# Performance work log

Measured on AMD Instinct MI355X. Metric: run time of the kernel, lower is better.

## Reference

```python
import jax, jax.numpy as jnp
import numpy as np

# --- constants (match init_kwargs / input_specs) ---
N_NODES = 32768   # total nodes
N_EDGES = 262144  # total edges (avg degree 8)
B = 512           # number of graphs
D = 64            # node feature / hidden dim (scalar irreps width)
DE = 16           # edge attribute dim
NEXP = 8          # num_experts
K = 2             # top-k


def setup_inputs() -> dict:
    key = jax.random.key(0)
    ks = jax.random.split(key, 20)
    x = jax.random.normal(ks[0], (N_NODES, D), dtype=jnp.float32)
    edge_src = jax.random.randint(ks[1], (N_EDGES,), 0, N_NODES, dtype=jnp.int32)
    edge_dst = jax.random.randint(ks[2], (N_EDGES,), 0, N_NODES, dtype=jnp.int32)
    edge_attr = jax.random.normal(ks[3], (N_EDGES, DE), dtype=jnp.float32)
    # sorted graph ids, every graph non-empty (64 nodes each)
    batch = jnp.repeat(jnp.arange(B, dtype=jnp.int32), N_NODES // B)
    s = 1.0 / np.sqrt(D)
    se = 1.0 / np.sqrt(DE)
    # embedding GNN params
    emb_We = jax.random.normal(ks[4], (DE, D), dtype=jnp.float32) * se
    emb_W1 = jax.random.normal(ks[5], (D, D), dtype=jnp.float32) * s
    emb_W2 = jax.random.normal(ks[6], (D, D), dtype=jnp.float32) * s
    emb_b = jnp.zeros((D,), dtype=jnp.float32)
    # gating network
    Wg = jax.random.normal(ks[7], (D, NEXP), dtype=jnp.float32) * s
    bg = jnp.zeros((NEXP,), dtype=jnp.float32)
    # stacked expert params [NEXP, ...]
    ex_We = jax.random.normal(ks[8], (NEXP, DE, D), dtype=jnp.float32) * se
    ex_W1 = jax.random.normal(ks[9], (NEXP, D, D), dtype=jnp.float32) * s
    ex_W2 = jax.random.normal(ks[10], (NEXP, D, D), dtype=jnp.float32) * s
    ex_b = jnp.zeros((NEXP, D), dtype=jnp.float32)
    ex_Wout = jax.random.normal(ks[11], (NEXP, D, 1), dtype=jnp.float32) * s
    ex_bout = jnp.zeros((NEXP, 1), dtype=jnp.float32)
    return {
        "x": x, "edge_attr": edge_attr,
        "emb_We": emb_We, "emb_W1": emb_W1, "emb_W2": emb_W2, "emb_b": emb_b,
        "Wg": Wg, "bg": bg,
        "ex_We": ex_We, "ex_W1": ex_W1, "ex_W2": ex_W2, "ex_b": ex_b,
        "ex_Wout": ex_Wout, "ex_bout": ex_bout,
        "edge_src": edge_src, "edge_dst": edge_dst, "batch": batch,
    }


def _gnn_embed(x, edge_attr, We, W1, W2, b, src, dst, batch):
    # edge-gated messages: gather x[src], modulate by projected edge attrs, scatter to dst
    msg = x[src] * (edge_attr @ We)                          # [E, D]
    agg = jax.ops.segment_sum(msg, dst, num_segments=N_NODES)  # [N, D]
    h = jax.nn.relu(x @ W1 + agg @ W2 + b)                   # [N, D]
    # mean pooling per graph
    gsum = jax.ops.segment_sum(h, batch, num_segments=B)      # [B, D]
    cnt = jax.ops.segment_sum(jnp.ones((N_NODES, 1), h.dtype), batch, num_segments=B)
    return gsum / jnp.maximum(cnt, 1.0)                      # [B, D]


def _expert(x, edge_attr, We, W1, W2, b, Wout, bout, src, dst, batch):
    emb = _gnn_embed(x, edge_attr, We, W1, W2, b, src, dst, batch)
    return emb @ Wout + bout                                  # [B, 1]


def reference(x, edge_attr, emb_We, emb_W1, emb_W2, emb_b, Wg, bg,
              ex_We, ex_W1, ex_W2, ex_b, ex_Wout, ex_bout,
              edge_src, edge_dst, batch):
    # 1) graph embeddings via embedding GNN
    graph_emb = _gnn_embed(x, edge_attr, emb_We, emb_W1, emb_W2, emb_b,
                           edge_src, edge_dst, batch)          # [B, D]
    # 2) gating: softmax over experts, top-k, renormalize
    routing_weights = jax.nn.softmax(graph_emb @ Wg + bg, axis=1)  # [B, NEXP]
    top_k_weights, top_k_indices = jax.lax.top_k(routing_weights, K)
    norm_top_k = jax.nn.softmax(top_k_weights, axis=1)             # [B, K]
    # 3) dispatch: run every expert on the full batch (vectorized equivalent of
    #    the per-expert masked sub-batch loop), then gather routed outputs
    expert_outs = jax.vmap(
        lambda We, W1, W2, b, Wo, bo: _expert(
            x, edge_attr, We, W1, W2, b, Wo, bo, edge_src, edge_dst, batch)
    )(ex_We, ex_W1, ex_W2, ex_b, ex_Wout, ex_bout)             # [NEXP, B, 1]
    per_graph = expert_outs[:, :, 0].T                         # [B, NEXP]
    gathered = jnp.take_along_axis(per_graph, top_k_indices, axis=1)  # [B, K]
    # 4) weighted combine
    final_output = jnp.sum(gathered * norm_top_k, axis=1, keepdims=True)  # [B, 1]
    return final_output, routing_weights
```

## Files before the change

### kernel.cpp

```cpp
#include <hip/hip_runtime.h>

#define N_NODES 32768
#define N_EDGES 262144
#define NB      512
#define D       64
#define DE      16
#define NEXP    8

typedef __attribute__((ext_vector_type(8))) short  short8v;
typedef __attribute__((ext_vector_type(4))) float  floatx4;

static __device__ __forceinline__ unsigned short f2bf(float f) {
  unsigned int u = __float_as_uint(f);
  u += 0x7FFFu + ((u >> 16) & 1u);
  return (unsigned short)(u >> 16);
}


__global__ void hist_kernel(const int* __restrict__ dst, int* __restrict__ counts) {
  int i = blockIdx.x * blockDim.x + threadIdx.x;
  if (i < N_EDGES) atomicAdd(&counts[dst[i]], 1);
}

__global__ void scan1_kernel(const int* __restrict__ counts, int* __restrict__ offsets,
                             int* __restrict__ bsums) {
  __shared__ int sm[256];
  int t = threadIdx.x, i = blockIdx.x * 256 + t;
  int v = counts[i];
  sm[t] = v;
  __syncthreads();
  for (int off = 1; off < 256; off <<= 1) {
    int u = (t >= off) ? sm[t - off] : 0;
    __syncthreads();
    sm[t] += u;
    __syncthreads();
  }
  offsets[i] = sm[t] - v;
  if (t == 255) bsums[blockIdx.x] = sm[255];
}

__global__ void scan2_kernel(int* __restrict__ bsums) {
  __shared__ int sm[128];
  int t = threadIdx.x;
  int v = bsums[t];
  sm[t] = v;
  __syncthreads();
  for (int off = 1; off < 128; off <<= 1) {
    int u = (t >= off) ? sm[t - off] : 0;
    __syncthreads();
    sm[t] += u;
    __syncthreads();
  }
  bsums[t] = sm[t] - v;
}

__global__ void scan3_kernel(int* __restrict__ offsets, const int* __restrict__ bsums,
                             int* __restrict__ cursor) {
  int i = blockIdx.x * 256 + threadIdx.x;
  int v = offsets[i] + bsums[blockIdx.x];
  offsets[i] = v;
  cursor[i]  = v;
  if (i == 0) offsets[N_NODES] = N_EDGES;
}

__global__ void scatter_kernel(const int* __restrict__ dst, const int* __restrict__ src,
                               const float4* __restrict__ ea4, int* __restrict__ cursor,
                               int* __restrict__ sorted_src, float4* __restrict__ sea4,
                               const float* __restrict__ ex_W1, const float* __restrict__ ex_W2,
                               unsigned short* __restrict__ wpk) {
  int i = blockIdx.x * blockDim.x + threadIdx.x;
  if (i < N_EDGES) {
    int p = atomicAdd(&cursor[dst[i]], 1);
    sorted_src[p] = src[i];
    float4 a = ea4[(size_t)i * 4 + 0];
    float4 b = ea4[(size_t)i * 4 + 1];
    float4 c = ea4[(size_t)i * 4 + 2];
    float4 d = ea4[(size_t)i * 4 + 3];
    sea4[(size_t)p * 4 + 0] = a;
    sea4[(size_t)p * 4 + 1] = b;
    sea4[(size_t)p * 4 + 2] = c;
    sea4[(size_t)p * 4 + 3] = d;
  }
  if (i < NEXP * 2 * D * D) {
    int je  = i >> 13;
    int rem = i & 8191;
    int mat = rem >> 12;
    int cd  = rem & 4095;
    int col = cd >> 6, k = cd & 63;
    const float* W = mat ? ex_W2 : ex_W1;
    wpk[i] = f2bf(W[je * 4096 + k * 64 + col]);
  }
}


__global__ __launch_bounds__(256) void tkern(
    const float* __restrict__ x, const int* __restrict__ sorted_src,
    const float4* __restrict__ sea4, const int* __restrict__ offsets,
    const float* __restrict__ emb_We, float* __restrict__ agg0,
    unsigned int* __restrict__ Tp) {
  int lane = threadIdx.x & 63;
  int wv = threadIdx.x >> 6;
  int n0 = blockIdx.x * 8 + wv * 2;
  int n1 = n0 + 1;
  int st0 = __builtin_amdgcn_readfirstlane(offsets[n0]);
  int en0 = __builtin_amdgcn_readfirstlane(offsets[n0 + 1]);
  int en1 = __builtin_amdgcn_readfirstlane(offsets[n1 + 1]);
  int b0 = st0, b1 = en0;

  float tk0[DE], tk1[DE];
#pragma unroll
  for (int k = 0; k < DE; ++k) { tk0[k] = 0.f; tk1[k] = 0.f; }

  while (b0 < en0 || b1 < en1) {
    int e00 = (b0     < N_EDGES - 1) ? b0     : N_EDGES - 1;
    int e01 = (b0 + 1 < N_EDGES - 1) ? b0 + 1 : N_EDGES - 1;
    int e10 = (b1     < N_EDGES - 1) ? b1     : N_EDGES - 1;
    int e11 = (b1 + 1 < N_EDGES - 1) ? b1 + 1 : N_EDGES - 1;
    float m00 = (b0     < en0) ? 1.f : 0.f;
    float m01 = (b0 + 1 < en0) ? 1.f : 0.f;
    float m10 = (b1     < en1) ? 1.f : 0.f;
    float m11 = (b1 + 1 < en1) ? 1.f : 0.f;
    int s00 = sorted_src[e00];
    int s01 = sorted_src[e01];
    int s10 = sorted_src[e10];
    int s11 = sorted_src[e11];
    const float4* p00 = sea4 + ((size_t)e00 << 2);
    const float4* p01 = sea4 + ((size_t)e01 << 2);
    const float4* p10 = sea4 + ((size_t)e10 << 2);
    const float4* p11 = sea4 + ((size_t)e11 << 2);
    float4 a0 = p00[0], a1 = p00[1], a2 = p00[2], a3 = p00[3];
    float4 c0 = p01[0], c1 = p01[1], c2 = p01[2], c3 = p01[3];
    float4 d0 = p10[0], d1 = p10[1], d2 = p10[2], d3 = p10[3];
    float4 f0 = p11[0], f1 = p11[1], f2 = p11[2], f3 = p11[3];
    float x00 = x[(size_t)s00 * D + lane] * m00;
    float x01 = x[(size_t)s01 * D + lane] * m01;
    float x10 = x[(size_t)s10 * D + lane] * m10;
    float x11 = x[(size_t)s11 * D + lane] * m11;

    tk0[0]  += x00 * a0.x; tk0[1]  += x00 * a0.y; tk0[2]  += x00 * a0.z; tk0[3]  += x00 * a0.w;
    tk0[4]  += x00 * a1.x; tk0[5]  += x00 * a1.y; tk0[6]  += x00 * a1.z; tk0[7]  += x00 * a1.w;
    tk0[8]  += x00 * a2.x; tk0[9]  += x00 * a2.y; tk0[10] += x00 * a2.z; tk0[11] += x00 * a2.w;
    tk0[12] += x00 * a3.x; tk0[13] += x00 * a3.y; tk0[14] += x00 * a3.z; tk0[15] += x00 * a3.w;
    tk0[0]  += x01 * c0.x; tk0[1]  += x01 * c0.y; tk0[2]  += x01 * c0.z; tk0[3]  += x01 * c0.w;
    tk0[4]  += x01 * c1.x; tk0[5]  += x01 * c1.y; tk0[6]  += x01 * c1.z; tk0[7]  += x01 * c1.w;
    tk0[8]  += x01 * c2.x; tk0[9]  += x01 * c2.y; tk0[10] += x01 * c2.z; tk0[11] += x01 * c2.w;
    tk0[12] += x01 * c3.x; tk0[13] += x01 * c3.y; tk0[14] += x01 * c3.z; tk0[15] += x01 * c3.w;
    tk1[0]  += x10 * d0.x; tk1[1]  += x10 * d0.y; tk1[2]  += x10 * d0.z; tk1[3]  += x10 * d0.w;
    tk1[4]  += x10 * d1.x; tk1[5]  += x10 * d1.y; tk1[6]  += x10 * d1.z; tk1[7]  += x10 * d1.w;
    tk1[8]  += x10 * d2.x; tk1[9]  += x10 * d2.y; tk1[10] += x10 * d2.z; tk1[11] += x10 * d2.w;
    tk1[12] += x10 * d3.x; tk1[13] += x10 * d3.y; tk1[14] += x10 * d3.z; tk1[15] += x10 * d3.w;
    tk1[0]  += x11 * f0.x; tk1[1]  += x11 * f0.y; tk1[2]  += x11 * f0.z; tk1[3]  += x11 * f0.w;
    tk1[4]  += x11 * f1.x; tk1[5]  += x11 * f1.y; tk1[6]  += x11 * f1.z; tk1[7]  += x11 * f1.w;
    tk1[8]  += x11 * f2.x; tk1[9]  += x11 * f2.y; tk1[10] += x11 * f2.z; tk1[11] += x11 * f2.w;
    tk1[12] += x11 * f3.x; tk1[13] += x11 * f3.y; tk1[14] += x11 * f3.z; tk1[15] += x11 * f3.w;
    b0 += 2; b1 += 2;
  }

  {
    float av0 = 0.f, av1 = 0.f;
#pragma unroll
    for (int k = 0; k < DE; ++k) {
      float ewk = emb_We[k * D + lane];
      av0 += tk0[k] * ewk;
      av1 += tk1[k] * ewk;
    }
    agg0[(size_t)n0 * D + lane] = av0;
    agg0[(size_t)n1 * D + lane] = av1;
  }
  unsigned int* tp0 = Tp + (size_t)n0 * (D * DE / 2) + lane;
  unsigned int* tp1 = Tp + (size_t)n1 * (D * DE / 2) + lane;
#pragma unroll
  for (int j = 0; j < 8; ++j) {
    unsigned int pk0 = (unsigned int)f2bf(tk0[2 * j]) |
                       ((unsigned int)f2bf(tk0[2 * j + 1]) << 16);
    unsigned int pk1 = (unsigned int)f2bf(tk1[2 * j]) |
                       ((unsigned int)f2bf(tk1[2 * j + 1]) << 16);
    tp0[(size_t)j * D] = pk0;
    tp1[(size_t)j * D] = pk1;
  }
}


__global__ __launch_bounds__(256) void gnn0_kernel(
    const float* __restrict__ x, const float* __restrict__ agg0,
    const float* __restrict__ W1, const float* __restrict__ W2,
    const float* __restrict__ bvv, float* __restrict__ graph_emb) {
  __shared__ __align__(16) float w1s[D * D];
  __shared__ __align__(16) float w2s[D * D];
  __shared__ __align__(16) float xs[D * D];
  __shared__ __align__(16) float as2[D * D];
  int b = blockIdx.x;
  int t = threadIdx.x;
  const float4* w1src = (const float4*)W1;
  const float4* w2src = (const float4*)W2;
  const float4* xsrc  = (const float4*)(x    + (size_t)b * D * D);
  const float4* asrc  = (const float4*)(agg0 + (size_t)b * D * D);
#pragma unroll
  for (int r = 0; r < 4; ++r) {
    ((float4*)w1s)[t + r * 256] = w1src[t + r * 256];
    ((float4*)w2s)[t + r * 256] = w2src[t + r * 256];
    ((float4*)xs)[t + r * 256]  = xsrc[t + r * 256];
    ((float4*)as2)[t + r * 256] = asrc[t + r * 256];
  }
  int w = t >> 6, lane = t & 63;
  float bias = bvv[lane];
  __syncthreads();
  float pool = 0.f;
#pragma unroll
  for (int q = 0; q < 4; ++q) {
    int n0 = w * 16 + q * 4;
    float a0 = bias, a1 = bias, a2 = bias, a3 = bias;
#pragma unroll 4
    for (int c4 = 0; c4 < 16; ++c4) {
      float4 x0 = *(const float4*)&xs[(n0 + 0) * D + c4 * 4];
      float4 x1 = *(const float4*)&xs[(n0 + 1) * D + c4 * 4];
      float4 x2 = *(const float4*)&xs[(n0 + 2) * D + c4 * 4];
      float4 x3 = *(const float4*)&xs[(n0 + 3) * D + c4 * 4];
      float4 g0 = *(const float4*)&as2[(n0 + 0) * D + c4 * 4];
      float4 g1 = *(const float4*)&as2[(n0 + 1) * D + c4 * 4];
      float4 g2 = *(const float4*)&as2[(n0 + 2) * D + c4 * 4];
      float4 g3 = *(const float4*)&as2[(n0 + 3) * D + c4 * 4];
      float w10 = w1s[(c4 * 4 + 0) * D + lane];
      float w11 = w1s[(c4 * 4 + 1) * D + lane];
      float w12 = w1s[(c4 * 4 + 2) * D + lane];
      float w13 = w1s[(c4 * 4 + 3) * D + lane];
      float w20 = w2s[(c4 * 4 + 0) * D + lane];
      float w21 = w2s[(c4 * 4 + 1) * D + lane];
      float w22 = w2s[(c4 * 4 + 2) * D + lane];
      float w23 = w2s[(c4 * 4 + 3) * D + lane];
      a0 += x0.x * w10 + x0.y * w11 + x0.z * w12 + x0.w * w13
          + g0.x * w20 + g0.y * w21 + g0.z * w22 + g0.w * w23;
      a1 += x1.x * w10 + x1.y * w11 + x1.z * w12 + x1.w * w13
          + g1.x * w20 + g1.y * w21 + g1.z * w22 + g1.w * w23;
      a2 += x2.x * w10 + x2.y * w11 + x2.z * w12 + x2.w * w13
          + g2.x * w20 + g2.y * w21 + g2.z * w22 + g2.w * w23;
      a3 += x3.x * w10 + x3.y * w11 + x3.z * w12 + x3.w * w13
          + g3.x * w20 + g3.y * w21 + g3.z * w22 + g3.w * w23;
    }
    pool += fmaxf(a0, 0.f) + fmaxf(a1, 0.f) + fmaxf(a2, 0.f) + fmaxf(a3, 0.f);
  }
  __syncthreads();
  xs[w * D + lane] = pool;
  __syncthreads();
  if (w == 0) {
    float s = xs[lane] + xs[D + lane] + xs[2 * D + lane] + xs[3 * D + lane];
    graph_emb[b * D + lane] = s * (1.f / 64.f);
  }
}


__global__ __launch_bounds__(512) void expert_kernel(
    const float* __restrict__ x, const unsigned int* __restrict__ Tp,
    const float* __restrict__ ex_We, const unsigned short* __restrict__ wpk,
    const float* __restrict__ ex_b, const float* __restrict__ ex_Wout,
    const float* __restrict__ ex_bout,
    const float* __restrict__ graph_emb, const float* __restrict__ Wg,
    const float* __restrict__ bg, float* __restrict__ out) {
  __shared__ __align__(16) short xls[4096];
  __shared__ __align__(16) short als[NEXP * 4096];
  __shared__ float pg[NEXP];
  __shared__ float lg[NEXP];
  int g = blockIdx.x;
  int t = threadIdx.x;
  {
    const float4* xp = (const float4*)(x + (size_t)g * 4096 + (size_t)t * 8);
    float4 va = xp[0], vb = xp[1];
    short8v pk;
    pk[0] = (short)f2bf(va.x); pk[1] = (short)f2bf(va.y);
    pk[2] = (short)f2bf(va.z); pk[3] = (short)f2bf(va.w);
    pk[4] = (short)f2bf(vb.x); pk[5] = (short)f2bf(vb.y);
    pk[6] = (short)f2bf(vb.z); pk[7] = (short)f2bf(vb.w);
    int row = t >> 3, slot = t & 7;
    *(short8v*)((char*)xls + (((row << 3) + (slot ^ (row & 7))) << 4)) = pk;
  }

  int je = t >> 6;
  int lane = t & 63;

  {
    float wr[DE];
#pragma unroll
    for (int k = 0; k < DE; ++k) wr[k] = ex_We[(size_t)je * DE * D + k * D + lane];
    char* abase = (char*)als + (size_t)je * 8192;
    int slot = lane >> 3;
    int within = (lane & 7) << 1;
    for (int i = 0; i < D; i += 2) {
      int nA = g * D + i, nB = nA + 1;
      const unsigned int* ta = Tp + (size_t)nA * 512 + lane;
      const unsigned int* tb = Tp + (size_t)nB * 512 + lane;
      unsigned int pa0 = ta[0],   pa1 = ta[64],  pa2 = ta[128], pa3 = ta[192];
      unsigned int pa4 = ta[256], pa5 = ta[320], pa6 = ta[384], pa7 = ta[448];
      unsigned int pb0 = tb[0],   pb1 = tb[64],  pb2 = tb[128], pb3 = tb[192];
      unsigned int pb4 = tb[256], pb5 = tb[320], pb6 = tb[384], pb7 = tb[448];
      float sA, sB;
      sA  = __uint_as_float(pa0 << 16)         * wr[0];
      sA += __uint_as_float(pa0 & 0xFFFF0000u) * wr[1];
      sA += __uint_as_float(pa1 << 16)         * wr[2];
      sA += __uint_as_float(pa1 & 0xFFFF0000u) * wr[3];
      sA += __uint_as_float(pa2 << 16)         * wr[4];
      sA += __uint_as_float(pa2 & 0xFFFF0000u) * wr[5];
      sA += __uint_as_float(pa3 << 16)         * wr[6];
      sA += __uint_as_float(pa3 & 0xFFFF0000u) * wr[7];
      sA += __uint_as_float(pa4 << 16)         * wr[8];
      sA += __uint_as_float(pa4 & 0xFFFF0000u) * wr[9];
      sA += __uint_as_float(pa5 << 16)         * wr[10];
      sA += __uint_as_float(pa5 & 0xFFFF0000u) * wr[11];
      sA += __uint_as_float(pa6 << 16)         * wr[12];
      sA += __uint_as_float(pa6 & 0xFFFF0000u) * wr[13];
      sA += __uint_as_float(pa7 << 16)         * wr[14];
      sA += __uint_as_float(pa7 & 0xFFFF0000u) * wr[15];
      sB  = __uint_as_float(pb0 << 16)         * wr[0];
      sB += __uint_as_float(pb0 & 0xFFFF0000u) * wr[1];
      sB += __uint_as_float(pb1 << 16)         * wr[2];
      sB += __uint_as_float(pb1 & 0xFFFF0000u) * wr[3];
      sB += __uint_as_float(pb2 << 16)         * wr[4];
      sB += __uint_as_float(pb2 & 0xFFFF0000u) * wr[5];
      sB += __uint_as_float(pb3 << 16)         * wr[6];
      sB += __uint_as_float(pb3 & 0xFFFF0000u) * wr[7];
      sB += __uint_as_float(pb4 << 16)         * wr[8];
      sB += __uint_as_float(pb4 & 0xFFFF0000u) * wr[9];
      sB += __uint_as_float(pb5 << 16)         * wr[10];
      sB += __uint_as_float(pb5 & 0xFFFF0000u) * wr[11];
      sB += __uint_as_float(pb6 << 16)         * wr[12];
      sB += __uint_as_float(pb6 & 0xFFFF0000u) * wr[13];
      sB += __uint_as_float(pb7 << 16)         * wr[14];
      sB += __uint_as_float(pb7 & 0xFFFF0000u) * wr[15];
      *(short*)(abase + (i    ) * 128 + ((slot ^ ( i      & 7)) << 4) + within) = (short)f2bf(sA);
      *(short*)(abase + (i + 1) * 128 + ((slot ^ ((i + 1) & 7)) << 4) + within) = (short)f2bf(sB);
    }
  }
  __syncthreads();

  int r = lane & 15, q = lane >> 4;
  const short* B1 = (const short*)(wpk + (size_t)je * 2 * 4096);
  const short* B2 = B1 + 4096;
  char* abase = (char*)als + (size_t)je * 8192;

  floatx4 acc[4][4];
#pragma unroll
  for (int i = 0; i < 4; ++i)
#pragma unroll
    for (int j = 0; j < 4; ++j) acc[i][j] = (floatx4){0.f, 0.f, 0.f, 0.f};

#pragma unroll
  for (int kk = 0; kk < 2; ++kk) {
    int ko = kk * 32 + q * 8;
    short8v af[4], bf[4];
#pragma unroll
    for (int rt = 0; rt < 4; ++rt) {
      int row = rt * 16 + r;
      int slot = kk * 4 + q;
      af[rt] = *(const short8v*)((char*)xls + (((row << 3) + (slot ^ (row & 7))) << 4));
    }
#pragma unroll
    for (int ct = 0; ct < 4; ++ct) bf[ct] = *(const short8v*)(B1 + (ct * 16 + r) * D + ko);
#pragma unroll
    for (int rt = 0; rt < 4; ++rt)
#pragma unroll
      for (int ct = 0; ct < 4; ++ct)
        acc[rt][ct] = __builtin_amdgcn_mfma_f32_16x16x32_bf16(af[rt], bf[ct], acc[rt][ct], 0, 0, 0);
  }
#pragma unroll
  for (int kk = 0; kk < 2; ++kk) {
    int ko = kk * 32 + q * 8;
    short8v af[4], bf[4];
#pragma unroll
    for (int rt = 0; rt < 4; ++rt) {
      int row = rt * 16 + r;
      int slot = kk * 4 + q;
      af[rt] = *(const short8v*)(abase + (row << 7) + ((slot ^ (row & 7)) << 4));
    }
#pragma unroll
    for (int ct = 0; ct < 4; ++ct) bf[ct] = *(const short8v*)(B2 + (ct * 16 + r) * D + ko);
#pragma unroll
    for (int rt = 0; rt < 4; ++rt)
#pragma unroll
      for (int ct = 0; ct < 4; ++ct)
        acc[rt][ct] = __builtin_amdgcn_mfma_f32_16x16x32_bf16(af[rt], bf[ct], acc[rt][ct], 0, 0, 0);
  }

  float o = 0.f;
#pragma unroll
  for (int ct = 0; ct < 4; ++ct) {
    float bcol = ex_b[je * D + ct * 16 + r];
    float s = 0.f;
#pragma unroll
    for (int rt = 0; rt < 4; ++rt)
#pragma unroll
      for (int rg = 0; rg < 4; ++rg) s += fmaxf(acc[rt][ct][rg] + bcol, 0.f);
    s += __shfl_xor(s, 16);
    s += __shfl_xor(s, 32);
    o += s * ex_Wout[je * D + ct * 16 + r];
  }
#pragma unroll
  for (int off = 8; off >= 1; off >>= 1) o += __shfl_xor(o, off);
  if (lane == 0) pg[je] = o * (1.f / 64.f) + ex_bout[je];
  __syncthreads();

  float* es = (float*)xls;
  if (t < 64) es[t] = graph_emb[g * D + t];
  __syncthreads();
  if (t < NEXP) {
    float v = bg[t];
    for (int d = 0; d < D; ++d) v += es[d] * Wg[d * NEXP + t];
    lg[t] = v;
  }
  __syncthreads();
  if (t < NEXP) {
    float l[NEXP];
    float mx = -1e30f;
#pragma unroll
    for (int e = 0; e < NEXP; ++e) { l[e] = lg[e]; mx = fmaxf(mx, l[e]); }
    float p[NEXP];
    float sum = 0.f;
#pragma unroll
    for (int e = 0; e < NEXP; ++e) { p[e] = expf(l[e] - mx); sum += p[e]; }
    float inv = 1.f / sum;
#pragma unroll
    for (int e = 0; e < NEXP; ++e) p[e] *= inv;
    out[NB + g * NEXP + t] = p[t];
    if (t == 0) {
      int i1 = -1; float v1 = -1e30f;
#pragma unroll
      for (int e = 0; e < NEXP; ++e) if (p[e] > v1) { v1 = p[e]; i1 = e; }
      int i2 = -1; float v2 = -1e30f;
#pragma unroll
      for (int e = 0; e < NEXP; ++e) if (e != i1 && p[e] > v2) { v2 = p[e]; i2 = e; }
      float rr = expf(v2 - v1);
      float n1 = 1.f / (1.f + rr);
      float n2 = rr / (1.f + rr);
      out[g] = n1 * pg[i1] + n2 * pg[i2];
    }
  }
}


extern "C" void kernel_launch(void* const* d_in, const int* in_sizes, int n_in,
                              void* d_out, int out_size, void* d_ws, size_t ws_size,
                              hipStream_t stream) {
  const float* x         = (const float*)d_in[0];
  const float* edge_attr = (const float*)d_in[1];
  const float* emb_We    = (const float*)d_in[2];
  const float* emb_W1    = (const float*)d_in[3];
  const float* emb_W2    = (const float*)d_in[4];
  const float* emb_b     = (const float*)d_in[5];
  const float* Wg        = (const float*)d_in[6];
  const float* bg        = (const float*)d_in[7];
  const float* ex_We     = (const float*)d_in[8];
  const float* ex_W1     = (const float*)d_in[9];
  const float* ex_W2     = (const float*)d_in[10];
  const float* ex_b      = (const float*)d_in[11];
  const float* ex_Wout   = (const float*)d_in[12];
  const float* ex_bout   = (const float*)d_in[13];
  const int* edge_src    = (const int*)d_in[14];
  const int* edge_dst    = (const int*)d_in[15];

  char* p = (char*)d_ws;
  auto alloc = [&](size_t bytes) {
    char* q = p;
    p += (bytes + 255) & ~(size_t)255;
    return q;
  };
  int*   counts     = (int*)alloc((size_t)N_NODES * 4);
  int*   offsets    = (int*)alloc((size_t)(N_NODES + 1) * 4);
  int*   cursor     = (int*)alloc((size_t)N_NODES * 4);
  int*   bsums      = (int*)alloc(128 * 4);
  int*   sorted_src = (int*)alloc((size_t)N_EDGES * 4);
  float* sorted_ea  = (float*)alloc((size_t)N_EDGES * DE * 4);
  unsigned int* Tp  = (unsigned int*)alloc((size_t)N_NODES * (D * DE / 2) * 4);
  float* agg0       = (float*)alloc((size_t)N_NODES * D * 4);
  unsigned short* wpk = (unsigned short*)alloc((size_t)NEXP * 2 * D * D * 2);
  float* graph_emb  = (float*)alloc((size_t)NB * D * 4);

  hipMemsetAsync(counts, 0, (size_t)N_NODES * 4, stream);
  hist_kernel<<<N_EDGES / 256, 256, 0, stream>>>(edge_dst, counts);
  scan1_kernel<<<N_NODES / 256, 256, 0, stream>>>(counts, offsets, bsums);
  scan2_kernel<<<1, 128, 0, stream>>>(bsums);
  scan3_kernel<<<N_NODES / 256, 256, 0, stream>>>(offsets, bsums, cursor);
  scatter_kernel<<<N_EDGES / 256, 256, 0, stream>>>(edge_dst, edge_src,
                                                    (const float4*)edge_attr, cursor,
                                                    sorted_src, (float4*)sorted_ea,
                                                    ex_W1, ex_W2, wpk);
  tkern<<<N_NODES / 8, 256, 0, stream>>>(x, sorted_src, (const float4*)sorted_ea,
                                         offsets, emb_We, agg0, Tp);
  gnn0_kernel<<<NB, 256, 0, stream>>>(x, agg0, emb_W1, emb_W2, emb_b, graph_emb);
  expert_kernel<<<NB, 512, 0, stream>>>(x, Tp, ex_We, wpk, ex_b, ex_Wout, ex_bout,
                                        graph_emb, Wg, bg, (float*)d_out);
}
```

Measured before the change: 210.2 us.

## Replace sorted edge-attr copy with permutation index; one node per wave in tkern

The scatter kernel stops copying 64-byte edge attribute rows into destination-sorted order and only records each edge's original index. tkern gathers edge_attr indirectly through that index, which removes a full write and re-read of the 16 MB attribute array. tkern also changes from two nodes per wave to one node per wave, unrolled four edges deep, with a launch-bounds occupancy hint. The trade-off is random 64-byte gathers from edge_attr and an extra index load per edge in the aggregation loop.

```diff
diff --git a/kernel.cpp b/kernel.cpp
--- a/kernel.cpp
+++ b/kernel.cpp
@@ -64,22 +64,15 @@
 }
 
 __global__ void scatter_kernel(const int* __restrict__ dst, const int* __restrict__ src,
-                               const float4* __restrict__ ea4, int* __restrict__ cursor,
-                               int* __restrict__ sorted_src, float4* __restrict__ sea4,
+                               int* __restrict__ cursor,
+                               int* __restrict__ sorted_src, int* __restrict__ edge_order,
                                const float* __restrict__ ex_W1, const float* __restrict__ ex_W2,
                                unsigned short* __restrict__ wpk) {
   int i = blockIdx.x * blockDim.x + threadIdx.x;
   if (i < N_EDGES) {
     int p = atomicAdd(&cursor[dst[i]], 1);
     sorted_src[p] = src[i];
-    float4 a = ea4[(size_t)i * 4 + 0];
-    float4 b = ea4[(size_t)i * 4 + 1];
-    float4 c = ea4[(size_t)i * 4 + 2];
-    float4 d = ea4[(size_t)i * 4 + 3];
-    sea4[(size_t)p * 4 + 0] = a;
-    sea4[(size_t)p * 4 + 1] = b;
-    sea4[(size_t)p * 4 + 2] = c;
-    sea4[(size_t)p * 4 + 3] = d;
+    edge_order[p] = i;
   }
   if (i < NEXP * 2 * D * D) {
     int je  = i >> 13;
@@ -93,90 +86,76 @@
 }
 
 
-__global__ __launch_bounds__(256) void tkern(
+__global__ __launch_bounds__(256, 4) void tkern(
     const float* __restrict__ x, const int* __restrict__ sorted_src,
-    const float4* __restrict__ sea4, const int* __restrict__ offsets,
-    const float* __restrict__ emb_We, float* __restrict__ agg0,
-    unsigned int* __restrict__ Tp) {
+    const int* __restrict__ edge_order, const float* __restrict__ edge_attr,
+    const int* __restrict__ offsets, const float* __restrict__ emb_We,
+    float* __restrict__ agg0, unsigned int* __restrict__ Tp) {
   int lane = threadIdx.x & 63;
   int wv = threadIdx.x >> 6;
-  int n0 = blockIdx.x * 8 + wv * 2;
-  int n1 = n0 + 1;
-  int st0 = __builtin_amdgcn_readfirstlane(offsets[n0]);
-  int en0 = __builtin_amdgcn_readfirstlane(offsets[n0 + 1]);
-  int en1 = __builtin_amdgcn_readfirstlane(offsets[n1 + 1]);
-  int b0 = st0, b1 = en0;
-
-  float tk0[DE], tk1[DE];
-#pragma unroll
-  for (int k = 0; k < DE; ++k) { tk0[k] = 0.f; tk1[k] = 0.f; }
-
-  while (b0 < en0 || b1 < en1) {
-    int e00 = (b0     < N_EDGES - 1) ? b0     : N_EDGES - 1;
-    int e01 = (b0 + 1 < N_EDGES - 1) ? b0 + 1 : N_EDGES - 1;
-    int e10 = (b1     < N_EDGES - 1) ? b1     : N_EDGES - 1;
-    int e11 = (b1 + 1 < N_EDGES - 1) ? b1 + 1 : N_EDGES - 1;
-    float m00 = (b0     < en0) ? 1.f : 0.f;
-    float m01 = (b0 + 1 < en0) ? 1.f : 0.f;
-    float m10 = (b1     < en1) ? 1.f : 0.f;
-    float m11 = (b1 + 1 < en1) ? 1.f : 0.f;
-    int s00 = sorted_src[e00];
-    int s01 = sorted_src[e01];
-    int s10 = sorted_src[e10];
-    int s11 = sorted_src[e11];
-    const float4* p00 = sea4 + ((size_t)e00 << 2);
-    const float4* p01 = sea4 + ((size_t)e01 << 2);
-    const float4* p10 = sea4 + ((size_t)e10 << 2);
-    const float4* p11 = sea4 + ((size_t)e11 << 2);
-    float4 a0 = p00[0], a1 = p00[1], a2 = p00[2], a3 = p00[3];
-    float4 c0 = p01[0], c1 = p01[1], c2 = p01[2], c3 = p01[3];
-    float4 d0 = p10[0], d1 = p10[1], d2 = p10[2], d3 = p10[3];
-    float4 f0 = p11[0], f1 = p11[1], f2 = p11[2], f3 = p11[3];
-    float x00 = x[(size_t)s00 * D + lane] * m00;
-    float x01 = x[(size_t)s01 * D + lane] * m01;
-    float x10 = x[(size_t)s10 * D + lane] * m10;
-    float x11 = x[(size_t)s11 * D + lane] * m11;
-
-    tk0[0]  += x00 * a0.x; tk0[1]  += x00 * a0.y; tk0[2]  += x00 * a0.z; tk0[3]  += x00 * a0.w;
-    tk0[4]  += x00 * a1.x; tk0[5]  += x00 * a1.y; tk0[6]  += x00 * a1.z; tk0[7]  += x00 * a1.w;
-    tk0[8]  += x00 * a2.x; tk0[9]  += x00 * a2.y; tk0[10] += x00 * a2.z; tk0[11] += x00 * a2.w;
-    tk0[12] += x00 * a3.x; tk0[13] += x00 * a3.y; tk0[14] += x00 * a3.z; tk0[15] += x00 * a3.w;
-    tk0[0]  += x01 * c0.x; tk0[1]  += x01 * c0.y; tk0[2]  += x01 * c0.z; tk0[3]  += x01 * c0.w;
-    tk0[4]  += x01 * c1.x; tk0[5]  += x01 * c1.y; tk0[6]  += x01 * c1.z; tk0[7]  += x01 * c1.w;
-    tk0[8]  += x01 * c2.x; tk0[9]  += x01 * c2.y; tk0[10] += x01 * c2.z; tk0[11] += x01 * c2.w;
-    tk0[12] += x01 * c3.x; tk0[13] += x01 * c3.y; tk0[14] += x01 * c3.z; tk0[15] += x01 * c3.w;
-    tk1[0]  += x10 * d0.x; tk1[1]  += x10 * d0.y; tk1[2]  += x10 * d0.z; tk1[3]  += x10 * d0.w;
-    tk1[4]  += x10 * d1.x; tk1[5]  += x10 * d1.y; tk1[6]  += x10 * d1.z; tk1[7]  += x10 * d1.w;
-    tk1[8]  += x10 * d2.x; tk1[9]  += x10 * d2.y; tk1[10] += x10 * d2.z; tk1[11] += x10 * d2.w;
-    tk1[12] += x10 * d3.x; tk1[13] += x10 * d3.y; tk1[14] += x10 * d3.z; tk1[15] += x10 * d3.w;
-    tk1[0]  += x11 * f0.x; tk1[1]  += x11 * f0.y; tk1[2]  += x11 * f0.z; tk1[3]  += x11 * f0.w;
-    tk1[4]  += x11 * f1.x; tk1[5]  += x11 * f1.y; tk1[6]  += x11 * f1.z; tk1[7]  += x11 * f1.w;
-    tk1[8]  += x11 * f2.x; tk1[9]  += x11 * f2.y; tk1[10] += x11 * f2.z; tk1[11] += x11 * f2.w;
-    tk1[12] += x11 * f3.x; tk1[13] += x11 * f3.y; tk1[14] += x11 * f3.z; tk1[15] += x11 * f3.w;
-    b0 += 2; b1 += 2;
+  int n = blockIdx.x * 4 + wv;
+  int st = __builtin_amdgcn_readfirstlane(offsets[n]);
+  int en = __builtin_amdgcn_readfirstlane(offsets[n + 1]);
+
+  float tk[DE];
+#pragma unroll
+  for (int k = 0; k < DE; ++k) tk[k] = 0.f;
+
+  for (int b = st; b < en; b += 4) {
+    int e0 = b;
+    int e1 = (b + 1 < en) ? b + 1 : b;
+    int e2 = (b + 2 < en) ? b + 2 : b;
+    int e3 = (b + 3 < en) ? b + 3 : b;
+    float m1 = (b + 1 < en) ? 1.f : 0.f;
+    float m2 = (b + 2 < en) ? 1.f : 0.f;
+    float m3 = (b + 3 < en) ? 1.f : 0.f;
+    int s0 = sorted_src[e0], s1 = sorted_src[e1];
+    int s2 = sorted_src[e2], s3 = sorted_src[e3];
+    int o0 = edge_order[e0], o1 = edge_order[e1];
+    int o2 = edge_order[e2], o3 = edge_order[e3];
+    const float4* q0 = (const float4*)(edge_attr + (size_t)o0 * DE);
+    const float4* q1 = (const float4*)(edge_attr + (size_t)o1 * DE);
+    const float4* q2 = (const float4*)(edge_attr + (size_t)o2 * DE);
+    const float4* q3 = (const float4*)(edge_attr + (size_t)o3 * DE);
+    float4 a0 = q0[0], a1 = q0[1], a2 = q0[2], a3 = q0[3];
+    float4 c0 = q1[0], c1 = q1[1], c2 = q1[2], c3 = q1[3];
+    float4 d0 = q2[0], d1 = q2[1], d2 = q2[2], d3 = q2[3];
+    float4 f0 = q3[0], f1 = q3[1], f2 = q3[2], f3 = q3[3];
+    float x0 = x[(size_t)s0 * D + lane];
+    float x1 = x[(size_t)s1 * D + lane] * m1;
+    float x2 = x[(size_t)s2 * D + lane] * m2;
+    float x3 = x[(size_t)s3 * D + lane] * m3;
+
+    tk[0]  += x0 * a0.x; tk[1]  += x0 * a0.y; tk[2]  += x0 * a0.z; tk[3]  += x0 * a0.w;
+    tk[4]  += x0 * a1.x; tk[5]  += x0 * a1.y; tk[6]  += x0 * a1.z; tk[7]  += x0 * a1.w;
+    tk[8]  += x0 * a2.x; tk[9]  += x0 * a2.y; tk[10] += x0 * a2.z; tk[11] += x0 * a2.w;
+    tk[12] += x0 * a3.x; tk[13] += x0 * a3.y; tk[14] += x0 * a3.z; tk[15] += x0 * a3.w;
+    tk[0]  += x1 * c0.x; tk[1]  += x1 * c0.y; tk[2]  += x1 * c0.z; tk[3]  += x1 * c0.w;
+    tk[4]  += x1 * c1.x; tk[5]  += x1 * c1.y; tk[6]  += x1 * c1.z; tk[7]  += x1 * c1.w;
+    tk[8]  += x1 * c2.x; tk[9]  += x1 * c2.y; tk[10] += x1 * c2.z; tk[11] += x1 * c2.w;
+    tk[12] += x1 * c3.x; tk[13] += x1 * c3.y; tk[14] += x1 * c3.z; tk[15] += x1 * c3.w;
+    tk[0]  += x2 * d0.x; tk[1]  += x2 * d0.y; tk[2]  += x2 * d0.z; tk[3]  += x2 * d0.w;
+    tk[4]  += x2 * d1.x; tk[5]  += x2 * d1.y; tk[6]  += x2 * d1.z; tk[7]  += x2 * d1.w;
+    tk[8]  += x2 * d2.x; tk[9]  += x2 * d2.y; tk[10] += x2 * d2.z; tk[11] += x2 * d2.w;
+    tk[12] += x2 * d3.x; tk[13] += x2 * d3.y; tk[14] += x2 * d3.z; tk[15] += x2 * d3.w;
+    tk[0]  += x3 * f0.x; tk[1]  += x3 * f0.y; tk[2]  += x3 * f0.z; tk[3]  += x3 * f0.w;
+    tk[4]  += x3 * f1.x; tk[5]  += x3 * f1.y; tk[6]  += x3 * f1.z; tk[7]  += x3 * f1.w;
+    tk[8]  += x3 * f2.x; tk[9]  += x3 * f2.y; tk[10] += x3 * f2.z; tk[11] += x3 * f2.w;
+    tk[12] += x3 * f3.x; tk[13] += x3 * f3.y; tk[14] += x3 * f3.z; tk[15] += x3 * f3.w;
   }
 
   {
-    float av0 = 0.f, av1 = 0.f;
-#pragma unroll
-    for (int k = 0; k < DE; ++k) {
-      float ewk = emb_We[k * D + lane];
-      av0 += tk0[k] * ewk;
-      av1 += tk1[k] * ewk;
-    }
-    agg0[(size_t)n0 * D + lane] = av0;
-    agg0[(size_t)n1 * D + lane] = av1;
-  }
-  unsigned int* tp0 = Tp + (size_t)n0 * (D * DE / 2) + lane;
-  unsigned int* tp1 = Tp + (size_t)n1 * (D * DE / 2) + lane;
+    float a = 0.f;
+#pragma unroll
+    for (int k = 0; k < DE; ++k) a += tk[k] * emb_We[k * D + lane];
+    agg0[(size_t)n * D + lane] = a;
+  }
+  unsigned int* tp = Tp + (size_t)n * (D * DE / 2) + lane;
 #pragma unroll
   for (int j = 0; j < 8; ++j) {
-    unsigned int pk0 = (unsigned int)f2bf(tk0[2 * j]) |
-                       ((unsigned int)f2bf(tk0[2 * j + 1]) << 16);
-    unsigned int pk1 = (unsigned int)f2bf(tk1[2 * j]) |
-                       ((unsigned int)f2bf(tk1[2 * j + 1]) << 16);
-    tp0[(size_t)j * D] = pk0;
-    tp1[(size_t)j * D] = pk1;
+    unsigned int pk = (unsigned int)f2bf(tk[2 * j]) |
+                      ((unsigned int)f2bf(tk[2 * j + 1]) << 16);
+    tp[(size_t)j * D] = pk;
   }
 }
 
@@ -466,7 +445,7 @@
   int*   cursor     = (int*)alloc((size_t)N_NODES * 4);
   int*   bsums      = (int*)alloc(128 * 4);
   int*   sorted_src = (int*)alloc((size_t)N_EDGES * 4);
-  float* sorted_ea  = (float*)alloc((size_t)N_EDGES * DE * 4);
+  int*   edge_order = (int*)alloc((size_t)N_EDGES * 4);
   unsigned int* Tp  = (unsigned int*)alloc((size_t)N_NODES * (D * DE / 2) * 4);
   float* agg0       = (float*)alloc((size_t)N_NODES * D * 4);
   unsigned short* wpk = (unsigned short*)alloc((size_t)NEXP * 2 * D * D * 2);
@@ -477,11 +456,10 @@
   scan1_kernel<<<N_NODES / 256, 256, 0, stream>>>(counts, offsets, bsums);
   scan2_kernel<<<1, 128, 0, stream>>>(bsums);
   scan3_kernel<<<N_NODES / 256, 256, 0, stream>>>(offsets, bsums, cursor);
-  scatter_kernel<<<N_EDGES / 256, 256, 0, stream>>>(edge_dst, edge_src,
-                                                    (const float4*)edge_attr, cursor,
-                                                    sorted_src, (float4*)sorted_ea,
+  scatter_kernel<<<N_EDGES / 256, 256, 0, stream>>>(edge_dst, edge_src, cursor,
+                                                    sorted_src, edge_order,
                                                     ex_W1, ex_W2, wpk);
-  tkern<<<N_NODES / 8, 256, 0, stream>>>(x, sorted_src, (const float4*)sorted_ea,
+  tkern<<<N_NODES / 4, 256, 0, stream>>>(x, sorted_src, edge_order, edge_attr,
                                          offsets, emb_We, agg0, Tp);
   gnn0_kernel<<<NB, 256, 0, stream>>>(x, agg0, emb_W1, emb_W2, emb_b, graph_emb);
   expert_kernel<<<NB, 512, 0, stream>>>(x, Tp, ex_We, wpk, ex_b, ex_Wout, ex_bout,
```

Result: no change. 210.9 us (+0.3%).
